# Kernel tuning notes

Hardware: AMD Instinct MI355X
Metric: run time of the kernel (lower is better)

Reference implementation:

```python
import jax, jax.numpy as jnp
import numpy as np

N_HEAD = 16
D_HEAD = 64
D_MODEL = 1024
SCALE = 1.0 / float(D_HEAD) ** 0.5
LN_EPS = 1e-5


def _rel_shift(x):
    # x: [b, n, i, j] -> Transformer-XL relative shift
    b, n, i, j = x.shape
    x = jnp.pad(x, ((0, 0), (0, 0), (0, 0), (1, 0)))  # zero-pad front of last dim
    x = x.reshape(b, n, j + 1, i)[:, :, 1:, :]
    return x.reshape(b, n, i, j)


def _layer_norm(x, g, b):
    mu = jnp.mean(x, axis=-1, keepdims=True)
    var = jnp.mean(jnp.square(x - mu), axis=-1, keepdims=True)
    return g * (x - mu) / jnp.sqrt(var + LN_EPS) + b


def setup_inputs() -> dict:
    key = jax.random.key(0)
    ks = jax.random.split(key, 8)
    qlen, bsz = 1024, 4
    w = jax.random.normal(ks[0], (qlen, bsz, D_MODEL), jnp.float32)
    r = jax.random.normal(ks[1], (qlen, D_MODEL), jnp.float32)
    r_w_bias = 0.02 * jax.random.normal(ks[2], (N_HEAD, D_HEAD), jnp.float32)
    r_r_bias = 0.02 * jax.random.normal(ks[3], (N_HEAD, D_HEAD), jnp.float32)
    attn_mask = jnp.triu(jnp.ones((qlen, qlen), bool), 1)  # causal, True = masked
    qkv_w = 0.02 * jax.random.normal(ks[4], (D_MODEL, 3 * N_HEAD * D_HEAD), jnp.float32)
    qkv_b = jnp.zeros((3 * N_HEAD * D_HEAD,), jnp.float32)
    rk_w = 0.02 * jax.random.normal(ks[5], (D_MODEL, N_HEAD * D_HEAD), jnp.float32)
    rk_b = jnp.zeros((N_HEAD * D_HEAD,), jnp.float32)
    o_w = 0.02 * jax.random.normal(ks[6], (N_HEAD * D_HEAD, D_MODEL), jnp.float32)
    o_b = jnp.zeros((D_MODEL,), jnp.float32)
    ln_g = jnp.ones((D_MODEL,), jnp.float32)
    ln_b = jnp.zeros((D_MODEL,), jnp.float32)
    return {"w": w, "r": r, "r_w_bias": r_w_bias, "r_r_bias": r_r_bias,
            "qkv_w": qkv_w, "qkv_b": qkv_b, "rk_w": rk_w, "rk_b": rk_b,
            "o_w": o_w, "o_b": o_b, "ln_g": ln_g, "ln_b": ln_b,
            "attn_mask": attn_mask}


def reference(w, r, r_w_bias, r_r_bias, qkv_w, qkv_b, rk_w, rk_b, o_w, o_b, ln_g, ln_b, attn_mask):
    qlen, bsz, _ = w.shape
    # post-lnorm path (pre_lnorm=False)
    heads = w @ qkv_w + qkv_b                       # [q, b, 3*H*D]
    q, k, v = jnp.split(heads, 3, axis=-1)
    q = q.reshape(qlen, bsz, N_HEAD, D_HEAD)
    k = k.reshape(qlen, bsz, N_HEAD, D_HEAD)
    v = v.reshape(qlen, bsz, N_HEAD, D_HEAD)
    rk = (r @ rk_w + rk_b).reshape(-1, N_HEAD, D_HEAD)  # [rlen, H, D]
    AC = jnp.einsum('ibnd,jbnd->bnij', q + r_w_bias, k)
    BD = _rel_shift(jnp.einsum('ibnd,jnd->bnij', q + r_r_bias, rk))
    score = SCALE * (AC + BD)                       # [b, H, q, k]
    score = jnp.where(attn_mask[None, None, :, :], -jnp.inf, score)
    prob = jax.nn.softmax(score, axis=-1)
    vec = jnp.einsum('bnij,jbnd->ibnd', prob, v).reshape(qlen, bsz, N_HEAD * D_HEAD)
    attn_out = vec @ o_w + o_b
    return _layer_norm(w + attn_out, ln_g, ln_b)
```

## Files before the change

kernel.cpp:

```cpp
#include <hip/hip_runtime.h>
#include <math.h>

#define QL 1024
#define BSZ 4
#define NH 16
#define DH 64
#define DM 1024
#define SCALE_F 0.125f

typedef __attribute__((ext_vector_type(8))) short bf16x8;
typedef __attribute__((ext_vector_type(4))) float f32x4;

__device__ __forceinline__ unsigned short f2bf(float f) {
  union { float f; unsigned int u; } c; c.f = f;
  unsigned int u = c.u;
  u += 0x7FFFu + ((u >> 16) & 1u);
  return (unsigned short)(u >> 16);
}
__device__ __forceinline__ float bf2f(unsigned short u) {
  union { unsigned int i; float f; } c; c.i = ((unsigned int)u) << 16;
  return c.f;
}

__device__ __forceinline__ void ld_lds16(const unsigned short* g, unsigned short* l) {
  __builtin_amdgcn_global_load_lds(
      (const __attribute__((address_space(1))) unsigned int*)g,
      (__attribute__((address_space(3))) unsigned int*)l, 16, 0, 0);
}

__device__ __forceinline__ bf16x8 frag64(const unsigned short* lds, int n, int s) {
  return *(const bf16x8*)(lds + n * 64 + ((s ^ (n & 7)) * 8));
}

template <int CTRL>
__device__ __forceinline__ float dpp_mv(float x) {
  return __int_as_float(__builtin_amdgcn_update_dpp(
      0, __float_as_int(x), CTRL, 0xf, 0xf, true));
}
__device__ __forceinline__ float rowsum16(float x) {
  x += dpp_mv<0x121>(x);
  x += dpp_mv<0x122>(x);
  x += dpp_mv<0x124>(x);
  x += dpp_mv<0x128>(x);
  return x;
}

__global__ __launch_bounds__(256) void prep_kernel(
    const float* __restrict__ w, const float* __restrict__ r,
    const float* __restrict__ qkv_w, const float* __restrict__ rk_w,
    const float* __restrict__ o_w,
    unsigned short* __restrict__ wb, unsigned short* __restrict__ rb,
    unsigned short* __restrict__ qkv_wt, unsigned short* __restrict__ rk_wt,
    unsigned short* __restrict__ o_wt, float* __restrict__ drk) {
  __shared__ __align__(16) unsigned short t[64][72];
  const int bid = blockIdx.x, tid = threadIdx.x;
  if (bid >= 3840) {
    int idx = (bid - 3840) * 256 + tid;
    ((float4*)drk)[idx] = make_float4(0.f, 0.f, 0.f, 0.f);
    return;
  }
  if (bid < 2560) {
    const float* in = (bid < 2048) ? w : r;
    unsigned short* out = (bid < 2048) ? wb : rb;
    int idx = ((bid < 2048) ? bid : (bid - 2048)) * 256 + tid;
    float4 a = *(const float4*)(in + (size_t)idx * 8);
    float4 b = *(const float4*)(in + (size_t)idx * 8 + 4);
    unsigned short o[8] = {f2bf(a.x), f2bf(a.y), f2bf(a.z), f2bf(a.w),
                           f2bf(b.x), f2bf(b.y), f2bf(b.z), f2bf(b.w)};
    *(uint4*)(out + (size_t)idx * 8) = *(const uint4*)o;
    return;
  }
  const float* in; unsigned short* out; int N, n0, k0;
  if (bid < 3328) {
    int l = bid - 2560; in = qkv_w; out = qkv_wt; N = 3072;
    n0 = (l % 48) * 64; k0 = (l / 48) * 64;
  } else if (bid < 3584) {
    int l = bid - 3328; in = rk_w; out = rk_wt; N = 1024;
    n0 = (l & 15) * 64; k0 = (l >> 4) * 64;
  } else {
    int l = bid - 3584; in = o_w; out = o_wt; N = 1024;
    n0 = (l & 15) * 64; k0 = (l >> 4) * 64;
  }
  for (int f = tid; f < 1024; f += 256) {
    int rr = f >> 4, c4 = (f & 15) * 4;
    float4 v = *(const float4*)(in + (size_t)(k0 + rr) * N + n0 + c4);
    t[c4 + 0][rr] = f2bf(v.x); t[c4 + 1][rr] = f2bf(v.y);
    t[c4 + 2][rr] = f2bf(v.z); t[c4 + 3][rr] = f2bf(v.w);
  }
  __syncthreads();
  for (int f = tid; f < 512; f += 256) {
    int rr = f >> 3, seg = (f & 7) * 8;
    *(uint4*)(out + (size_t)(n0 + rr) * 1024 + k0 + seg) = *(const uint4*)&t[rr][seg];
  }
}

__global__ __launch_bounds__(512) void gemm12(
    const unsigned short* __restrict__ wb, const unsigned short* __restrict__ rb,
    const unsigned short* __restrict__ qkv_wt, const unsigned short* __restrict__ rk_wt,
    const float* __restrict__ qkv_b, const float* __restrict__ rk_b,
    const float* __restrict__ rwb, const float* __restrict__ rrb,
    unsigned short* __restrict__ qbf, unsigned short* __restrict__ kbf,
    unsigned short* __restrict__ vtb, unsigned short* __restrict__ rkbf,
    float* __restrict__ drk) {
  __shared__ __align__(16) unsigned short As[2 * 4096];
  __shared__ __align__(16) unsigned short Bs[2 * 8192];
  const int bid = blockIdx.x, tid = threadIdx.x;
  const int w = tid >> 6, lane = tid & 63;
  const int quad = lane >> 4, l15 = lane & 15;
  const int wr = w >> 2, wc = w & 3;
  const bool job0 = bid < 384;
  const unsigned short *A, *BT;
  const float* bias;
  int bm, bn;
  if (job0) {
    A = wb; BT = qkv_wt; bias = qkv_b;
    bn = (bid % 12) * 256; bm = (bid / 12) * 128;
  } else {
    int l = bid - 384;
    A = rb; BT = rk_wt; bias = rk_b;
    bn = (l & 3) * 256; bm = (l >> 2) * 128;
  }
  const int srow = tid >> 2;
  const int sseg = (tid & 3) ^ (srow & 3);
  f32x4 acc[4][4] = {};

  auto stage = [&](int bf, int k0) {
    ld_lds16(A + (size_t)(bm + srow) * 1024 + k0 + sseg * 8, As + bf * 4096 + w * 512);
#pragma unroll
    for (int i = 0; i < 2; ++i)
      ld_lds16(BT + (size_t)(bn + i * 128 + srow) * 1024 + k0 + sseg * 8,
               Bs + bf * 8192 + i * 4096 + w * 512);
  };

  int buf = 0;
  stage(0, 0);
  for (int k0 = 0; k0 < 1024; k0 += 32) {
    __syncthreads();
    if (k0 + 32 < 1024) stage(buf ^ 1, k0 + 32);
    const unsigned short* Al = As + buf * 4096;
    const unsigned short* Bl = Bs + buf * 8192;
    const int sa = quad ^ (l15 & 3);
    bf16x8 af[4], bfr[4];
#pragma unroll
    for (int rt = 0; rt < 4; ++rt)
      af[rt] = *(const bf16x8*)&Al[(wr * 64 + rt * 16 + l15) * 32 + sa * 8];
#pragma unroll
    for (int nt = 0; nt < 4; ++nt)
      bfr[nt] = *(const bf16x8*)&Bl[(wc * 64 + nt * 16 + l15) * 32 + sa * 8];
#pragma unroll
    for (int rt = 0; rt < 4; ++rt)
#pragma unroll
      for (int nt = 0; nt < 4; ++nt)
        acc[rt][nt] = __builtin_amdgcn_mfma_f32_16x16x32_bf16(af[rt], bfr[nt], acc[rt][nt], 0, 0, 0);
    buf ^= 1;
  }

  if (job0) {
#pragma unroll
    for (int rt = 0; rt < 4; ++rt)
#pragma unroll
      for (int nt = 0; nt < 4; ++nt) {
        int gc = bn + wc * 64 + nt * 16 + l15;
        float bv = bias[gc];
        int part = gc >> 10, h = (gc >> 6) & 15, d = gc & 63;
#pragma unroll
        for (int reg = 0; reg < 4; ++reg) {
          int gr = bm + wr * 64 + rt * 16 + quad * 4 + reg;
          float val = acc[rt][nt][reg] + bv;
          int i = gr >> 2, b = gr & 3;
          if (part == 0)
            qbf[((size_t)((b * NH + h) * QL + i)) * DH + d] = f2bf(val);
          else if (part == 1)
            kbf[((size_t)((b * NH + h) * QL + i)) * DH + d] = f2bf(val);
          else
            vtb[((size_t)((b * NH + h) * DH + d)) * QL + i] = f2bf(val);
        }
      }
  } else {
    const int h = (bn + wc * 64) >> 6;
    float df[4];
#pragma unroll
    for (int nt = 0; nt < 4; ++nt) {
      int dd = nt * 16 + l15;
      df[nt] = rrb[h * DH + dd] - rwb[h * DH + dd];
    }
#pragma unroll
    for (int rt = 0; rt < 4; ++rt) {
      float s[4] = {0.f, 0.f, 0.f, 0.f};
#pragma unroll
      for (int nt = 0; nt < 4; ++nt) {
        int d = nt * 16 + l15;
        float bv = bias[h * DH + d];
#pragma unroll
        for (int reg = 0; reg < 4; ++reg) {
          int gr = bm + wr * 64 + rt * 16 + quad * 4 + reg;
          float val = acc[rt][nt][reg] + bv;
          rkbf[((size_t)(h * QL + gr)) * DH + d] = f2bf(val);
          s[reg] += val * df[nt];
        }
      }
#pragma unroll
      for (int reg = 0; reg < 4; ++reg) {
        float v = s[reg];
        v += __shfl_xor(v, 1);
        v += __shfl_xor(v, 2);
        v += __shfl_xor(v, 4);
        v += __shfl_xor(v, 8);
        if (l15 == 0) {
          int j = bm + wr * 64 + rt * 16 + quad * 4 + reg;
          atomicAdd(&drk[h * QL + j], v);
        }
      }
    }
  }
}

__global__ __launch_bounds__(512) void gemm_o(
    const unsigned short* __restrict__ A, const unsigned short* __restrict__ BT,
    const float* __restrict__ bias, float* __restrict__ Cf) {
  __shared__ __align__(16) unsigned short As[2 * 4096];
  __shared__ __align__(16) unsigned short Bs[2 * 2048];
  const int tid = threadIdx.x;
  const int w = tid >> 6, lane = tid & 63;
  const int quad = lane >> 4, l15 = lane & 15;
  const int wr = w >> 1, wc = w & 1;
  const int bm = blockIdx.y * 128, bn = blockIdx.x * 64;
  const int srow = w * 16 + (lane >> 2);
  const int sseg = (lane & 3) ^ ((lane >> 2) & 3);
  f32x4 acc[2][2] = {};

  auto stage = [&](int bf, int k0) {
    ld_lds16(A + (size_t)(bm + srow) * 1024 + k0 + sseg * 8, As + bf * 4096 + w * 512);
    if (w < 4)
      ld_lds16(BT + (size_t)(bn + srow) * 1024 + k0 + sseg * 8, Bs + bf * 2048 + w * 512);
  };

  int buf = 0;
  stage(0, 0);
  for (int k0 = 0; k0 < 1024; k0 += 32) {
    __syncthreads();
    if (k0 + 32 < 1024) stage(buf ^ 1, k0 + 32);
    const unsigned short* Al = As + buf * 4096;
    const unsigned short* Bl = Bs + buf * 2048;
    const int sa = quad ^ (l15 & 3);
    bf16x8 af[2], bfr[2];
#pragma unroll
    for (int rt = 0; rt < 2; ++rt)
      af[rt] = *(const bf16x8*)&Al[(wr * 32 + rt * 16 + l15) * 32 + sa * 8];
#pragma unroll
    for (int nt = 0; nt < 2; ++nt)
      bfr[nt] = *(const bf16x8*)&Bl[(wc * 32 + nt * 16 + l15) * 32 + sa * 8];
#pragma unroll
    for (int rt = 0; rt < 2; ++rt)
#pragma unroll
      for (int nt = 0; nt < 2; ++nt)
        acc[rt][nt] = __builtin_amdgcn_mfma_f32_16x16x32_bf16(af[rt], bfr[nt], acc[rt][nt], 0, 0, 0);
    buf ^= 1;
  }

#pragma unroll
  for (int rt = 0; rt < 2; ++rt)
#pragma unroll
    for (int nt = 0; nt < 2; ++nt) {
      int gc = bn + wc * 32 + nt * 16 + l15;
      float bv = bias[gc];
#pragma unroll
      for (int reg = 0; reg < 4; ++reg) {
        int gr = bm + wr * 32 + rt * 16 + quad * 4 + reg;
        Cf[(size_t)gr * DM + gc] = acc[rt][nt][reg] + bv;
      }
    }
}

__global__ __launch_bounds__(256, 4) void attn_kernel(
    const unsigned short* __restrict__ qbf, const unsigned short* __restrict__ kbf,
    const unsigned short* __restrict__ vtb, const unsigned short* __restrict__ rkb,
    const float* __restrict__ drk, const float* __restrict__ rwb,
    unsigned short* __restrict__ vecb) {
  __shared__ __align__(16) unsigned short SH[20480];
  unsigned short* Ks = SH;
  unsigned short* Vs = SH + 8192;
  unsigned short* PM = SH + 16384;

  const int tid = threadIdx.x;
  const int wg = tid >> 6, lane = tid & 63;
  const int quad = lane >> 4, l15 = lane & 15;
  const int bh = blockIdx.x, b = bh >> 4, h = bh & 15;
  const int y = 15 - (int)blockIdx.y;
  const int i0 = y * 64, tS = y, T = y + 1;

  const unsigned short* kB0 = kbf + (size_t)bh * QL * DH;
  const unsigned short* vB0 = vtb + (size_t)bh * DH * QL;
  const unsigned short* rB0 = rkb + (size_t)h * QL * DH;
  const float* drkh = drk + h * QL;
  unsigned short* pmw = PM + wg * 1024;

  const int srow8 = lane >> 3, sseg8 = lane & 7;

  bf16x8 qf[2];
  {
    int qrow = i0 + wg * 16 + l15;
    const unsigned short* qp = qbf + ((size_t)bh * QL + qrow) * DH;
#pragma unroll
    for (int s = 0; s < 2; ++s) {
      int off = s * 32 + quad * 8;
      uint4 raw = *(const uint4*)(qp + off);
      const unsigned short* ru = (const unsigned short*)&raw;
      float4 wb0 = *(const float4*)(rwb + h * DH + off);
      float4 wb1 = *(const float4*)(rwb + h * DH + off + 4);
      union { bf16x8 v; unsigned short u[8]; } qc;
      qc.u[0] = f2bf(bf2f(ru[0]) + wb0.x); qc.u[1] = f2bf(bf2f(ru[1]) + wb0.y);
      qc.u[2] = f2bf(bf2f(ru[2]) + wb0.z); qc.u[3] = f2bf(bf2f(ru[3]) + wb0.w);
      qc.u[4] = f2bf(bf2f(ru[4]) + wb1.x); qc.u[5] = f2bf(bf2f(ru[5]) + wb1.y);
      qc.u[6] = f2bf(bf2f(ru[6]) + wb1.z); qc.u[7] = f2bf(bf2f(ru[7]) + wb1.w);
      qf[s] = qc.v;
    }
  }

  auto rel_frag = [&](int gb, f32x4& c) {
    int row = min(gb + l15, QL - 1);
    const unsigned short* rp = rB0 + (size_t)row * DH;
    f32x4 a = {0.f, 0.f, 0.f, 0.f};
    a = __builtin_amdgcn_mfma_f32_16x16x32_bf16(qf[0], *(const bf16x8*)(rp + quad * 8), a, 0, 0, 0);
    a = __builtin_amdgcn_mfma_f32_16x16x32_bf16(qf[1], *(const bf16x8*)(rp + 32 + quad * 8), a, 0, 0, 0);
    float dv = drkh[row];
    a[0] += dv; a[1] += dv; a[2] += dv; a[3] += dv;
    c = a;
  };

  auto stage_tile = [&](int t, int buf) {
    const unsigned short* kb = kB0 + (size_t)(t * 64) * DH;
    const unsigned short* vb = vB0 + t * 64;
    unsigned short* kd = Ks + buf * 4096;
    unsigned short* vd = Vs + buf * 4096;
#pragma unroll
    for (int ii = 0; ii < 2; ++ii) {
      int row = wg * 16 + ii * 8 + srow8;
      int gs = sseg8 ^ (row & 7);
      ld_lds16(kb + (size_t)row * DH + gs * 8, kd + (wg * 16 + ii * 8) * 64);
      ld_lds16(vb + (size_t)row * QL + gs * 8, vd + (wg * 16 + ii * 8) * 64);
    }
  };

  float lrow[4] = {0.f, 0.f, 0.f, 0.f};
  f32x4 pv[4];
#pragma unroll
  for (int r = 0; r < 4; ++r) pv[r] = (f32x4){0.f, 0.f, 0.f, 0.f};

  f32x4 rc[5];
  {
    const int Bt0 = 1008 - i0 - 16 * wg;
#pragma unroll
    for (int f = 0; f < 5; ++f) rel_frag(Bt0 + 16 * f, rc[f]);
  }

  int buf = 0;
  stage_tile(0, 0);
  for (int t = 0; t < T; ++t) {
    __syncthreads();
    if (t + 1 < T) stage_tile(t + 1, buf ^ 1);
    const bool diag = (t == tS);
    const unsigned short* ksl = Ks + buf * 4096;
    const unsigned short* vsl = Vs + buf * 4096;

    f32x4 sacc[4];
#pragma unroll
    for (int nt = 0; nt < 4; ++nt) {
      int n = nt * 16 + l15;
      f32x4 c = {0.f, 0.f, 0.f, 0.f};
      c = __builtin_amdgcn_mfma_f32_16x16x32_bf16(qf[0], frag64(ksl, n, quad), c, 0, 0, 0);
      c = __builtin_amdgcn_mfma_f32_16x16x32_bf16(qf[1], frag64(ksl, n, 4 + quad), c, 0, 0, 0);
      sacc[nt] = c;
    }

#pragma unroll
    for (int r = 0; r < 4; ++r) {
      const int il = wg * 16 + quad * 4 + r;
      const int ls = l15 + 15 - quad * 4 - r;
      const int srcl = (quad << 4) | (ls & 15);
      float rot[5];
#pragma unroll
      for (int f = 0; f < 5; ++f) rot[f] = __shfl(rc[f][r], srcl, 64);
      const bool lo = ls < 16;
      float psum = 0.f;
      const int prow = quad * 4 + r;
      const int psw = prow & 7;
#pragma unroll
      for (int nt = 0; nt < 4; ++nt) {
        float band = lo ? rot[nt] : rot[nt + 1];
        float s = (sacc[nt][r] + band) * SCALE_F;
        if (diag && (nt * 16 + l15) > il) s = -1e30f;
        float e = __expf(s);
        psum += e;
        int jl = nt * 16 + l15;
        pmw[prow * 64 + (((jl >> 3) ^ psw) << 3) + (jl & 7)] = f2bf(e);
      }
      lrow[r] += rowsum16(psum);
    }

    bf16x8 pf0 = frag64(pmw, l15, quad);
    bf16x8 pf1 = frag64(pmw, l15, 4 + quad);
#pragma unroll
    for (int nt = 0; nt < 4; ++nt) {
      int n = nt * 16 + l15;
      pv[nt] = __builtin_amdgcn_mfma_f32_16x16x32_bf16(pf0, frag64(vsl, n, quad), pv[nt], 0, 0, 0);
      pv[nt] = __builtin_amdgcn_mfma_f32_16x16x32_bf16(pf1, frag64(vsl, n, 4 + quad), pv[nt], 0, 0, 0);
    }

    if (t + 1 < T) {
      rc[0] = rc[4];
      const int Bt = 1008 - i0 + 64 * (t + 1) - 16 * wg;
#pragma unroll
      for (int f = 1; f < 5; ++f) rel_frag(Bt + 16 * f, rc[f]);
    }
    buf ^= 1;
  }

#pragma unroll
  for (int nt = 0; nt < 4; ++nt)
#pragma unroll
    for (int r = 0; r < 4; ++r) {
      int il = wg * 16 + quad * 4 + r;
      float val = pv[nt][r] / lrow[r];
      vecb[((size_t)((i0 + il) * BSZ + b)) * DM + h * DH + nt * 16 + l15] = f2bf(val);
    }
}

__global__ __launch_bounds__(256) void ln_kernel(
    const float* __restrict__ w, const float* __restrict__ attn,
    const float* __restrict__ g, const float* __restrict__ bta,
    float* __restrict__ out) {
  __shared__ float red[4];
  __shared__ float sval[2];
  const int row = blockIdx.x, tid = threadIdx.x;
  const float* wr = w + (size_t)row * DM;
  const float* ar = attn + (size_t)row * DM;
  float4 wv = *(const float4*)(wr + tid * 4);
  float4 av = *(const float4*)(ar + tid * 4);
  float x0 = wv.x + av.x, x1 = wv.y + av.y, x2 = wv.z + av.z, x3 = wv.w + av.w;
  float s = x0 + x1 + x2 + x3;
#pragma unroll
  for (int off = 32; off; off >>= 1) s += __shfl_down(s, off, 64);
  const int lane = tid & 63, wvi = tid >> 6;
  if (lane == 0) red[wvi] = s;
  __syncthreads();
  if (tid == 0) sval[0] = (red[0] + red[1] + red[2] + red[3]) * (1.0f / 1024.0f);
  __syncthreads();
  const float mu = sval[0];
  float d0 = x0 - mu, d1 = x1 - mu, d2 = x2 - mu, d3 = x3 - mu;
  float vs2 = d0 * d0 + d1 * d1 + d2 * d2 + d3 * d3;
#pragma unroll
  for (int off = 32; off; off >>= 1) vs2 += __shfl_down(vs2, off, 64);
  if (lane == 0) red[wvi] = vs2;
  __syncthreads();
  if (tid == 0)
    sval[1] = rsqrtf((red[0] + red[1] + red[2] + red[3]) * (1.0f / 1024.0f) + 1e-5f);
  __syncthreads();
  const float inv = sval[1];
  float4 gv = *(const float4*)(g + tid * 4);
  float4 bv = *(const float4*)(bta + tid * 4);
  float4 ov;
  ov.x = gv.x * d0 * inv + bv.x;
  ov.y = gv.y * d1 * inv + bv.y;
  ov.z = gv.z * d2 * inv + bv.z;
  ov.w = gv.w * d3 * inv + bv.w;
  *(float4*)(out + (size_t)row * DM + tid * 4) = ov;
}

extern "C" void kernel_launch(void* const* d_in, const int* in_sizes, int n_in,
                              void* d_out, int out_size, void* d_ws, size_t ws_size,
                              hipStream_t stream) {
  const float* w     = (const float*)d_in[0];
  const float* r     = (const float*)d_in[1];
  const float* rwb   = (const float*)d_in[2];
  const float* rrb   = (const float*)d_in[3];
  const float* qkv_w = (const float*)d_in[4];
  const float* qkv_b = (const float*)d_in[5];
  const float* rk_w  = (const float*)d_in[6];
  const float* rk_b  = (const float*)d_in[7];
  const float* o_w   = (const float*)d_in[8];
  const float* o_b   = (const float*)d_in[9];
  const float* ln_g  = (const float*)d_in[10];
  const float* ln_b  = (const float*)d_in[11];

  float* out = (float*)d_out;
  char* p = (char*)d_ws;
  unsigned short* wb     = (unsigned short*)p; p += (size_t)4096 * 1024 * 2;
  unsigned short* rb     = (unsigned short*)p; p += (size_t)1024 * 1024 * 2;
  unsigned short* qkv_wt = (unsigned short*)p; p += (size_t)3072 * 1024 * 2;
  unsigned short* rk_wt  = (unsigned short*)p; p += (size_t)1024 * 1024 * 2;
  unsigned short* o_wt   = (unsigned short*)p; p += (size_t)1024 * 1024 * 2;
  unsigned short* qbf    = (unsigned short*)p; p += (size_t)BSZ * NH * QL * DH * 2;
  unsigned short* kbf    = (unsigned short*)p; p += (size_t)BSZ * NH * QL * DH * 2;
  unsigned short* vtb    = (unsigned short*)p; p += (size_t)BSZ * NH * QL * DH * 2;
  unsigned short* rkbf   = (unsigned short*)p; p += (size_t)NH * QL * DH * 2;
  float*          drk    = (float*)p;          p += (size_t)NH * QL * 4;
  unsigned short* vecb   = (unsigned short*)p; p += (size_t)4096 * 1024 * 2;
  float*          attnf  = (float*)p;          p += (size_t)4096 * 1024 * 4;

  prep_kernel<<<3856, 256, 0, stream>>>(w, r, qkv_w, rk_w, o_w,
                                        wb, rb, qkv_wt, rk_wt, o_wt, drk);
  gemm12<<<416, 512, 0, stream>>>(wb, rb, qkv_wt, rk_wt, qkv_b, rk_b, rwb, rrb,
                                  qbf, kbf, vtb, rkbf, drk);
  attn_kernel<<<dim3(64, 16), 256, 0, stream>>>(qbf, kbf, vtb, rkbf, drk, rwb, vecb);
  gemm_o<<<dim3(16, 32), 512, 0, stream>>>(vecb, o_wt, o_b, attnf);
  ln_kernel<<<4096, 256, 0, stream>>>(w, attnf, ln_g, ln_b, out);
}
```

Baseline: 275.8 us.

## Split causal attention key range into chunks with separate combine kernel

```diff
diff --git a/kernel.cpp b/kernel.cpp
--- a/kernel.cpp
+++ b/kernel.cpp
@@ -44,6 +44,26 @@
   x += dpp_mv<0x128>(x);
   return x;
 }
+
+__device__ const unsigned char c_tab[40] = {
+  60, 61, 62, 63,
+  56, 57, 58,
+  52, 53, 54,
+  48, 49, 50,
+  44, 45, 46,
+  40, 41,
+  36, 37,
+  32, 33,
+  28, 29,
+  24, 20, 16, 12,
+  8, 25, 42, 59,
+  4, 21, 38, 55,
+  0, 17, 34, 51};
+__device__ const unsigned char c_inv[16][4] = {
+  {36, 0, 0, 0}, {32, 0, 0, 0}, {28, 0, 0, 0}, {27, 0, 0, 0},
+  {26, 37, 0, 0}, {25, 33, 0, 0}, {24, 29, 0, 0}, {22, 23, 0, 0},
+  {20, 21, 38, 0}, {18, 19, 34, 0}, {16, 17, 30, 0}, {13, 14, 15, 0},
+  {10, 11, 12, 39}, {7, 8, 9, 35}, {4, 5, 6, 31}, {0, 1, 2, 3}};
 
 __global__ __launch_bounds__(256) void prep_kernel(
     const float* __restrict__ w, const float* __restrict__ r,
@@ -276,7 +296,7 @@
     const unsigned short* __restrict__ qbf, const unsigned short* __restrict__ kbf,
     const unsigned short* __restrict__ vtb, const unsigned short* __restrict__ rkb,
     const float* __restrict__ drk, const float* __restrict__ rwb,
-    unsigned short* __restrict__ vecb) {
+    float* __restrict__ pvpart, float* __restrict__ lpart) {
   __shared__ __align__(16) unsigned short SH[20480];
   unsigned short* Ks = SH;
   unsigned short* Vs = SH + 8192;
@@ -285,9 +305,12 @@
   const int tid = threadIdx.x;
   const int wg = tid >> 6, lane = tid & 63;
   const int quad = lane >> 4, l15 = lane & 15;
-  const int bh = blockIdx.x, b = bh >> 4, h = bh & 15;
-  const int y = 15 - (int)blockIdx.y;
-  const int i0 = y * 64, tS = y, T = y + 1;
+  const int bh = blockIdx.x, h = bh & 15;
+  const int cid = blockIdx.y;
+  const int pk = c_tab[cid];
+  const int y = pk >> 2, ch = pk & 3;
+  const int i0 = y * 64, tS = y;
+  const int t0 = ch * 4, t1 = min(t0 + 4, y + 1);
 
   const unsigned short* kB0 = kbf + (size_t)bh * QL * DH;
   const unsigned short* vB0 = vtb + (size_t)bh * DH * QL;
@@ -349,16 +372,16 @@
 
   f32x4 rc[5];
   {
-    const int Bt0 = 1008 - i0 - 16 * wg;
+    const int Bt0 = 1008 - i0 + 64 * t0 - 16 * wg;
 #pragma unroll
     for (int f = 0; f < 5; ++f) rel_frag(Bt0 + 16 * f, rc[f]);
   }
 
   int buf = 0;
-  stage_tile(0, 0);
-  for (int t = 0; t < T; ++t) {
+  stage_tile(t0, 0);
+  for (int t = t0; t < t1; ++t) {
     __syncthreads();
-    if (t + 1 < T) stage_tile(t + 1, buf ^ 1);
+    if (t + 1 < t1) stage_tile(t + 1, buf ^ 1);
     const bool diag = (t == tS);
     const unsigned short* ksl = Ks + buf * 4096;
     const unsigned short* vsl = Vs + buf * 4096;
@@ -407,7 +430,7 @@
       pv[nt] = __builtin_amdgcn_mfma_f32_16x16x32_bf16(pf1, frag64(vsl, n, 4 + quad), pv[nt], 0, 0, 0);
     }
 
-    if (t + 1 < T) {
+    if (t + 1 < t1) {
       rc[0] = rc[4];
       const int Bt = 1008 - i0 + 64 * (t + 1) - 16 * wg;
 #pragma unroll
@@ -416,14 +439,44 @@
     buf ^= 1;
   }
 
+  float* slab = pvpart + ((size_t)(bh * 40 + cid) << 12);
+  float* lp = lpart + (size_t)(bh * 40 + cid) * 64;
 #pragma unroll
   for (int nt = 0; nt < 4; ++nt)
 #pragma unroll
     for (int r = 0; r < 4; ++r) {
       int il = wg * 16 + quad * 4 + r;
-      float val = pv[nt][r] / lrow[r];
-      vecb[((size_t)((i0 + il) * BSZ + b)) * DM + h * DH + nt * 16 + l15] = f2bf(val);
-    }
+      slab[il * 64 + nt * 16 + l15] = pv[nt][r];
+    }
+  if (l15 == 0) {
+#pragma unroll
+    for (int r = 0; r < 4; ++r) lp[wg * 16 + quad * 4 + r] = lrow[r];
+  }
+}
+
+__global__ __launch_bounds__(256) void attn_combine(
+    const float* __restrict__ pvpart, const float* __restrict__ lpart,
+    unsigned short* __restrict__ vecb) {
+  __shared__ float Linv[64];
+  const int bh = blockIdx.x, y = blockIdx.y, b = bh >> 4, h = bh & 15;
+  const int nc = (y >> 2) + 1;
+  const int tid = threadIdx.x;
+  if (tid < 64) {
+    float s = 0.f;
+    for (int c = 0; c < nc; ++c)
+      s += lpart[((size_t)bh * 40 + c_inv[y][c]) * 64 + tid];
+    Linv[tid] = 1.0f / s;
+  }
+  __syncthreads();
+#pragma unroll
+  for (int k = 0; k < 16; ++k) {
+    int idx = k * 256 + tid;
+    int rr = idx >> 6, cc = idx & 63;
+    float s = 0.f;
+    for (int c = 0; c < nc; ++c)
+      s += pvpart[(((size_t)bh * 40 + c_inv[y][c]) << 12) + idx];
+    vecb[((size_t)((y * 64 + rr) * BSZ + b)) * DM + h * DH + cc] = f2bf(s * Linv[rr]);
+  }
 }
 
 __global__ __launch_bounds__(256) void ln_kernel(
@@ -497,12 +550,16 @@
   float*          drk    = (float*)p;          p += (size_t)NH * QL * 4;
   unsigned short* vecb   = (unsigned short*)p; p += (size_t)4096 * 1024 * 2;
   float*          attnf  = (float*)p;          p += (size_t)4096 * 1024 * 4;
+  float*          pvpart = (float*)p;          p += (size_t)64 * 40 * 4096 * 4;
+  float*          lpart  = (float*)p;          p += (size_t)64 * 40 * 64 * 4;
 
   prep_kernel<<<3856, 256, 0, stream>>>(w, r, qkv_w, rk_w, o_w,
                                         wb, rb, qkv_wt, rk_wt, o_wt, drk);
   gemm12<<<416, 512, 0, stream>>>(wb, rb, qkv_wt, rk_wt, qkv_b, rk_b, rwb, rrb,
                                   qbf, kbf, vtb, rkbf, drk);
-  attn_kernel<<<dim3(64, 16), 256, 0, stream>>>(qbf, kbf, vtb, rkbf, drk, rwb, vecb);
+  attn_kernel<<<dim3(64, 40), 256, 0, stream>>>(qbf, kbf, vtb, rkbf, drk, rwb,
+                                                pvpart, lpart);
+  attn_combine<<<dim3(64, 16), 256, 0, stream>>>(pvpart, lpart, vecb);
   gemm_o<<<dim3(16, 32), 512, 0, stream>>>(vecb, o_wt, o_b, attnf);
   ln_kernel<<<4096, 256, 0, stream>>>(w, attnf, ln_g, ln_b, out);
 }
```

Measured after the change: 296.9 us. 7.6% more time.
